# Kernel tuning notes

Hardware: AMD Instinct MI355X
Metric: run time of the kernel (lower is better)

Reference implementation:

```python
import jax, jax.numpy as jnp
import numpy as np

IN_CH = 1024   # backbone channels
N_T = 81       # n_targets (COCO classes + bg)
K = 7          # PSROI grid size
H = 100        # feature map height
WID = 100      # feature map width
R = 1024       # number of regions
S = 2          # bilinear sampling points per bin edge (PSROIAlign-style average)


def setup_inputs() -> dict:
    key = jax.random.key(0)
    k1, k2, k3 = jax.random.split(key, 3)
    x = jax.random.normal(k1, (IN_CH, H, WID), dtype=jnp.float32)
    # regions: fractional (i, j, h, w) = (center_y, center_x, height, width) in [0,1]
    regions = jax.random.uniform(k2, (R, 4), dtype=jnp.float32)
    conv_w = jax.random.normal(k3, (N_T * K * K, IN_CH), dtype=jnp.float32) * 0.02
    conv_b = jnp.zeros((N_T * K * K,), dtype=jnp.float32)
    return {"x": x, "regions": regions, "conv_w": conv_w, "conv_b": conv_b}


def _bilinear_pool(map_thw, ys, xs):
    """Average of bilinear samples of one bin's score map.

    map_thw: (T, H, W) score map for this (u, v) bin's channel group.
    ys: (R, S) sample row coords.  xs: (R, S) sample col coords.
    Returns (R, T): per-region average-pooled bin value.
    """
    Hm, Wm = map_thw.shape[1], map_thw.shape[2]
    ys = jnp.clip(ys, 0.0, Hm - 1)
    xs = jnp.clip(xs, 0.0, Wm - 1)
    y0 = jnp.floor(ys)
    x0 = jnp.floor(xs)
    y0i = y0.astype(jnp.int32)
    x0i = x0.astype(jnp.int32)
    y1i = jnp.minimum(y0i + 1, Hm - 1)
    x1i = jnp.minimum(x0i + 1, Wm - 1)
    wy1 = ys - y0
    wy0 = 1.0 - wy1
    wx1 = xs - x0
    wx0 = 1.0 - wx1

    def g(yi, xi):  # gather (T, R, S, S)
        return map_thw[:, yi[:, :, None], xi[:, None, :]]

    v = (g(y0i, x0i) * (wy0[:, :, None] * wx0[:, None, :])
         + g(y0i, x1i) * (wy0[:, :, None] * wx1[:, None, :])
         + g(y1i, x0i) * (wy1[:, :, None] * wx0[:, None, :])
         + g(y1i, x1i) * (wy1[:, :, None] * wx1[:, None, :]))
    return v.mean((2, 3)).T  # (R, T)


def reference(x, regions, conv_w, conv_b):
    # 1x1 conv score map: (n_targets*k^2, H, W)
    sm = jnp.einsum('oc,chw->ohw', conv_w, x) + conv_b[:, None, None]
    sm = sm.reshape(N_T, K, K, H, WID)  # (T, ky, kx, H, W) position-sensitive groups

    # region geometry (fractional center/size -> absolute feature-map coords)
    top = (regions[:, 0] - regions[:, 2] * 0.5) * H     # (R,)
    left = (regions[:, 1] - regions[:, 3] * 0.5) * WID  # (R,)
    bh = regions[:, 2] * H / K                          # bin height
    bw = regions[:, 3] * WID / K                        # bin width

    off = (jnp.arange(S, dtype=jnp.float32) + 0.5) / S  # (S,) sample offsets in bin
    bins = jnp.arange(K, dtype=jnp.float32)             # (K,)
    ys = top[:, None, None] + (bins[None, :, None] + off[None, None, :]) * bh[:, None, None]   # (R,K,S)
    xs = left[:, None, None] + (bins[None, :, None] + off[None, None, :]) * bw[:, None, None]  # (R,K,S)

    # vmap over the k x k position-sensitive bins; bin (u,v) reads channel group (:,u,v)
    inner = jax.vmap(_bilinear_pool, in_axes=(1, None, 1))  # over kx: sm axis, xs axis
    outer = jax.vmap(inner, in_axes=(1, 1, None))           # over ky: sm axis, ys axis
    pooled = outer(sm, ys, xs)  # (K, K, R, T)

    # pooled.mean(-1).mean(-1) over the k x k grid
    scores = pooled.mean((0, 1))  # (R, T)
    return scores
```

## Files before the change

### kernel.cpp

```cpp
#include <hip/hip_runtime.h>
#include <cstddef>

#define IN_CH 1024
#define NT    81
#define KGRID 7
#define NBINS 49
#define HH    100
#define WW    100
#define NPIX  (HH*WW)
#define NREG  1024
#define COLB  82
#define NCOL  (NBINS*COLB)
#define NPADW 4096
#define SBIN  84
#define SROWB (NBINS*SBIN)
#define NG    8
#define NSC   2560
#define PXB   ((NPIX + 31) / 32)
#define PXG   (PXB * (IN_CH / 128))
#define PREPG (PXG + NPADW)

typedef unsigned short ushortT;
typedef short bf16x8 __attribute__((ext_vector_type(8)));
typedef float f32x4  __attribute__((ext_vector_type(4)));

static __device__ __forceinline__ unsigned short f2bf(float f) {
    unsigned int u = __builtin_bit_cast(unsigned int, f);
    return (unsigned short)((u + 0x7fffu + ((u >> 16) & 1u)) >> 16);
}

static __device__ __forceinline__ void gld_lds16(const ushortT* g, ushortT* l) {
    __builtin_amdgcn_global_load_lds(
        (__attribute__((address_space(1))) void*)(unsigned long long)(uintptr_t)g,
        (__attribute__((address_space(3))) void*)(unsigned int)(unsigned long long)(uintptr_t)l,
        16, 0, 0);
}

__global__ __launch_bounds__(256) void prep_fused(const float* __restrict__ x,
                                                  ushortT* __restrict__ xbT,
                                                  const float* __restrict__ conv_w,
                                                  ushortT* __restrict__ Wr) {
    __shared__ float tile[128][33];
    const int tid = threadIdx.x;
    const int bid = blockIdx.x;
    if (bid < PXG) {
        const int p0 = (bid % PXB) * 32;
        const int c0 = (bid / PXB) * 128;
        const int pl = tid & 31;
        const int cg = tid >> 5;
        const int p = p0 + pl;
#pragma unroll
        for (int it = 0; it < 16; ++it) {
            const int c = it * 8 + cg;
            tile[c][pl] = (p < NPIX) ? x[(size_t)(c0 + c) * NPIX + p] : 0.0f;
        }
        __syncthreads();
#pragma unroll
        for (int pass = 0; pass < 2; ++pass) {
            const int pix = pass * 16 + (tid >> 4);
            const int cb  = (tid & 15) * 8;
            if (p0 + pix < NPIX) {
                uint4 pk;
                pk.x = (unsigned int)f2bf(tile[cb + 0][pix]) | ((unsigned int)f2bf(tile[cb + 1][pix]) << 16);
                pk.y = (unsigned int)f2bf(tile[cb + 2][pix]) | ((unsigned int)f2bf(tile[cb + 3][pix]) << 16);
                pk.z = (unsigned int)f2bf(tile[cb + 4][pix]) | ((unsigned int)f2bf(tile[cb + 5][pix]) << 16);
                pk.w = (unsigned int)f2bf(tile[cb + 6][pix]) | ((unsigned int)f2bf(tile[cb + 7][pix]) << 16);
                *(uint4*)(xbT + (size_t)(p0 + pix) * IN_CH + c0 + cb) = pk;
            }
        }
    } else {
        const int row = bid - PXG;
        const int bin = row / COLB;
        const int t   = row - bin * COLB;
        const int c   = tid * 4;
        uint2 pk; pk.x = 0; pk.y = 0;
        if (bin < NBINS && t < NT) {
            const float4 v = *(const float4*)(conv_w + ((size_t)(t * NBINS + bin)) * IN_CH + c);
            pk.x = (unsigned int)f2bf(v.x) | ((unsigned int)f2bf(v.y) << 16);
            pk.y = (unsigned int)f2bf(v.z) | ((unsigned int)f2bf(v.w) << 16);
        }
        *(uint2*)(Wr + (size_t)row * IN_CH + c) = pk;
    }
}

__global__ __launch_bounds__(256) void gemm_sm(const ushortT* __restrict__ xbT,
                                               const ushortT* __restrict__ Wr,
                                               unsigned char* __restrict__ sm,
                                               float* __restrict__ scales) {
    __shared__ ushortT a_lds[128 * 32];
    __shared__ ushortT b_lds[128 * 32];
    const int tid  = threadIdx.x;
    const int lane = tid & 63;
    const int w    = tid >> 6;
    const int wm   = w & 1;
    const int wn   = w >> 1;
    const int n0   = blockIdx.x * 128;
    const int p0   = blockIdx.y * 128;

    const int srow0 = w * 32 + (lane >> 2);
    const int scol  = (lane & 3) * 8;
    int ap0 = p0 + srow0;      if (ap0 > NPIX - 1) ap0 = NPIX - 1;
    int ap1 = p0 + srow0 + 16; if (ap1 > NPIX - 1) ap1 = NPIX - 1;
    const ushortT* ag0 = xbT + (size_t)ap0 * IN_CH + scol;
    const ushortT* ag1 = xbT + (size_t)ap1 * IN_CH + scol;
    const ushortT* bg0 = Wr + (size_t)(n0 + srow0) * IN_CH + scol;
    const ushortT* bg1 = Wr + (size_t)(n0 + srow0 + 16) * IN_CH + scol;
    ushortT* al0 = a_lds + (w * 32) * 32;
    ushortT* al1 = a_lds + (w * 32 + 16) * 32;
    ushortT* bl0 = b_lds + (w * 32) * 32;
    ushortT* bl1 = b_lds + (w * 32 + 16) * 32;

    const int m_lane = lane & 15;
    const int k0     = (lane >> 4) * 8;

    f32x4 acc[4][4];
#pragma unroll
    for (int mt = 0; mt < 4; ++mt)
#pragma unroll
        for (int nt = 0; nt < 4; ++nt) acc[mt][nt] = (f32x4){0.f, 0.f, 0.f, 0.f};

    for (int kc = 0; kc < IN_CH / 32; ++kc) {
        __syncthreads();
        gld_lds16(ag0, al0);
        gld_lds16(ag1, al1);
        gld_lds16(bg0, bl0);
        gld_lds16(bg1, bl1);
        ag0 += 32; ag1 += 32; bg0 += 32; bg1 += 32;
        __syncthreads();

        bf16x8 af[4], bf[4];
#pragma unroll
        for (int mt = 0; mt < 4; ++mt)
            af[mt] = *(const bf16x8*)(a_lds + (wm * 64 + mt * 16 + m_lane) * 32 + k0);
#pragma unroll
        for (int nt = 0; nt < 4; ++nt)
            bf[nt] = *(const bf16x8*)(b_lds + (wn * 64 + nt * 16 + m_lane) * 32 + k0);
#pragma unroll
        for (int mt = 0; mt < 4; ++mt)
#pragma unroll
            for (int nt = 0; nt < 4; ++nt)
                acc[mt][nt] = __builtin_amdgcn_mfma_f32_16x16x32_bf16(af[mt], bf[nt], acc[mt][nt], 0, 0, 0);
    }

    float am = 0.0f;
#pragma unroll
    for (int mt = 0; mt < 4; ++mt)
#pragma unroll
        for (int nt = 0; nt < 4; ++nt)
#pragma unroll
            for (int rg = 0; rg < 4; ++rg)
                am = fmaxf(am, fabsf(acc[mt][nt][rg]));
    __syncthreads();
    float* red = (float*)a_lds;
    red[tid] = am;
    __syncthreads();
#pragma unroll
    for (int s = 128; s > 0; s >>= 1) {
        if (tid < s) red[tid] = fmaxf(red[tid], red[tid + s]);
        __syncthreads();
    }
    const float amax = fmaxf(red[0], 1e-30f);
    const float inv  = 127.0f / amax;
    if (tid == 0) scales[blockIdx.y * 32 + blockIdx.x] = amax * (1.0f / 127.0f);

    const int prow_base = p0 + wm * 64 + (lane >> 4) * 4;
    const int ncol_base = n0 + wn * 64 + m_lane;
    int  coloff[4];
    bool cok[4];
#pragma unroll
    for (int nt = 0; nt < 4; ++nt) {
        const int n = ncol_base + nt * 16;
        cok[nt] = (n < NCOL);
        coloff[nt] = n + 2 * (n / COLB);
    }
#pragma unroll
    for (int mt = 0; mt < 4; ++mt) {
#pragma unroll
        for (int rg = 0; rg < 4; ++rg) {
            const int p = prow_base + mt * 16 + rg;
            if (p < NPIX) {
                unsigned char* rowp = sm + (size_t)p * SROWB;
#pragma unroll
                for (int nt = 0; nt < 4; ++nt)
                    if (cok[nt]) {
                        const int q = __float2int_rn(acc[mt][nt][rg] * inv);
                        rowp[coloff[nt]] = (unsigned char)(signed char)q;
                    }
            }
        }
    }
}

__global__ __launch_bounds__(256) void pool_kernel(const unsigned char* __restrict__ sm,
                                                   const float* __restrict__ scales,
                                                   const float* __restrict__ regions,
                                                   const float* __restrict__ conv_b,
                                                   float* __restrict__ out) {
    __shared__ int   rowo[28]; __shared__ float roww[28];
    __shared__ int   coli[28]; __shared__ float colw[28];
    __shared__ int   pofs[120];
    __shared__ float pw[120];
    __shared__ int   pptb[120];
    __shared__ int   pnb[120];
    __shared__ float part[40][100];
    const int tid = threadIdx.x;
    const int r = blockIdx.x;
    const int g = blockIdx.y;

    if (tid < 28) {
        const float4 reg = *(const float4*)(regions + (size_t)r * 4);
        const float top = (reg.x - reg.z * 0.5f) * (float)HH;
        const float bh  = reg.z * ((float)HH / (float)KGRID);
        const int u = tid >> 2, i = tid & 3;
        const int s = i >> 1, hi = i & 1;
        float y = top + ((float)u + ((float)s + 0.5f) * 0.5f) * bh;
        y = fminf(fmaxf(y, 0.0f), (float)(HH - 1));
        const float y0f = floorf(y);
        const int y0 = (int)y0f;
        const float wy1 = y - y0f;
        rowo[tid] = (hi ? min(y0 + 1, HH - 1) : y0) * WW;
        roww[tid] = hi ? wy1 : (1.0f - wy1);
    } else if (tid >= 32 && tid < 60) {
        const float4 reg = *(const float4*)(regions + (size_t)r * 4);
        const float left = (reg.y - reg.w * 0.5f) * (float)WW;
        const float bw   = reg.w * ((float)WW / (float)KGRID);
        const int idx = tid - 32;
        const int v = idx >> 2, j = idx & 3;
        const int s = j >> 1, hi = j & 1;
        float xx = left + ((float)v + ((float)s + 0.5f) * 0.5f) * bw;
        xx = fminf(fmaxf(xx, 0.0f), (float)(WW - 1));
        const float x0f = floorf(xx);
        const int x0 = (int)x0f;
        const float wx1 = xx - x0f;
        coli[idx] = hi ? min(x0 + 1, WW - 1) : x0;
        colw[idx] = hi ? wx1 : (1.0f - wx1);
    }
    __syncthreads();
    if (tid < 120) {
        if (tid < 98) {
            const int tt = g * 98 + tid;
            const int bin = tt >> 4, tap = tt & 15;
            const int u = bin / KGRID, v = bin - u * KGRID;
            const int i = tap >> 2, j = tap & 3;
            const int pix = rowo[u * 4 + i] + coli[v * 4 + j];
            pofs[tid] = pix * SROWB + bin * SBIN;
            pw[tid]   = roww[u * 4 + i] * colw[v * 4 + j] * (1.0f / 196.0f);
            pptb[tid] = (pix >> 7) * 32;
            pnb[tid]  = bin * COLB;
        } else {
            pofs[tid] = 0;
            pw[tid]   = 0.0f;
            pptb[tid] = 0;
            pnb[tid]  = 0;
        }
    }
    __syncthreads();

    const int lane = tid & 63, w = tid >> 6;
    const int sub  = lane / 6;
    const int cg   = lane - sub * 6;
    if (sub < 10) {
        const int str = w * 10 + sub;
        uint4 v[3];
#pragma unroll
        for (int it = 0; it < 3; ++it)
            v[it] = *(const uint4*)(sm + pofs[it * 40 + str] + cg * 16);

        float acc[16];
#pragma unroll
        for (int ch = 0; ch < 16; ++ch) acc[ch] = 0.0f;
#pragma unroll
        for (int it = 0; it < 3; ++it) {
            const int l  = it * 40 + str;
            const float wt = pw[l];
            const int nb  = pnb[l] + cg * 16;
            const int nt0 = nb >> 7;
            const int rr  = nb & 127;
            const float s0 = scales[pptb[l] + nt0];
            const float s1 = scales[pptb[l] + nt0 + 1];
            const float w0 = wt * s0, w1 = wt * s1;
            const unsigned int uu[4] = {v[it].x, v[it].y, v[it].z, v[it].w};
#pragma unroll
            for (int b = 0; b < 4; ++b) {
#pragma unroll
                for (int k = 0; k < 4; ++k) {
                    const int ch = b * 4 + k;
                    const int q = (int)(signed char)((uu[b] >> (k * 8)) & 0xff);
                    acc[ch] += ((rr < 128 - ch) ? w0 : w1) * (float)q;
                }
            }
        }
#pragma unroll
        for (int b = 0; b < 4; ++b) {
            float4 p4;
            p4.x = acc[b * 4]; p4.y = acc[b * 4 + 1];
            p4.z = acc[b * 4 + 2]; p4.w = acc[b * 4 + 3];
            *(float4*)&part[str][cg * 16 + b * 4] = p4;
        }
    }
    __syncthreads();
    if (tid < NT) {
        float vv = 0.f;
#pragma unroll
        for (int s = 0; s < 40; ++s) vv += part[s][tid];
        if (g == 0) {
            float bsum = 0.f;
            for (int bin = 0; bin < NBINS; ++bin) bsum += conv_b[tid * NBINS + bin];
            vv += bsum * (1.0f / (float)NBINS);
        }
        atomicAdd(out + (size_t)r * NT + tid, vv);
    }
}

__global__ __launch_bounds__(256) void xpose_kernel(const float* __restrict__ x,
                                                    float* __restrict__ xt) {
    __shared__ float tile[32][33];
    const int p0 = blockIdx.x * 32;
    const int c0 = blockIdx.y * 32;
    const int tx = threadIdx.x;
    const int ty = threadIdx.y;
#pragma unroll
    for (int k = 0; k < 32; k += 8) {
        const int p = p0 + tx;
        if (p < NPIX) tile[ty + k][tx] = x[(size_t)(c0 + ty + k) * NPIX + p];
    }
    __syncthreads();
#pragma unroll
    for (int k = 0; k < 32; k += 8) {
        const int p = p0 + ty + k;
        if (p < NPIX) xt[(size_t)p * IN_CH + (c0 + tx)] = tile[tx][ty + k];
    }
}

template <bool XPOSED>
__global__ __launch_bounds__(256) void psroi_kernel(
    const float* __restrict__ xsrc, const float* __restrict__ regions,
    const float* __restrict__ conv_w, const float* __restrict__ conv_b,
    float* __restrict__ out) {
    __shared__ float w_lds[32 * 96];
    __shared__ float g_lds[32 * 64];
    __shared__ int   rowoff[64][4];
    __shared__ float rowwf[64][4];
    __shared__ int   colidx[64][4];
    __shared__ float colwf[64][4];
    const int tid = threadIdx.x;
    const int bin = blockIdx.x >> 4;
    const int rg  = blockIdx.x & 15;
    const int u = bin / KGRID, v = bin % KGRID;
    const int r0 = rg * 64;
    if (tid < 64) {
        const float4 reg = *(const float4*)(regions + (size_t)(r0 + tid) * 4);
        const float top  = (reg.x - reg.z * 0.5f) * (float)HH;
        const float left = (reg.y - reg.w * 0.5f) * (float)WW;
        const float bh = reg.z * ((float)HH / (float)KGRID);
        const float bw = reg.w * ((float)WW / (float)KGRID);
        const float scale = 1.0f / 196.0f;
#pragma unroll
        for (int s = 0; s < 2; s++) {
            const float off = (s + 0.5f) * 0.5f;
            float yy = top + ((float)u + off) * bh;
            yy = fminf(fmaxf(yy, 0.0f), (float)(HH - 1));
            const float y0f = floorf(yy);
            const int y0 = (int)y0f;
            const float wy1 = yy - y0f;
            rowoff[tid][2 * s] = y0 * WW;
            rowoff[tid][2 * s + 1] = min(y0 + 1, HH - 1) * WW;
            rowwf[tid][2 * s] = (1.0f - wy1) * scale;
            rowwf[tid][2 * s + 1] = wy1 * scale;
            float xx = left + ((float)v + off) * bw;
            xx = fminf(fmaxf(xx, 0.0f), (float)(WW - 1));
            const float x0f = floorf(xx);
            const int x0 = (int)x0f;
            const float wx1 = xx - x0f;
            colidx[tid][2 * s] = x0;
            colidx[tid][2 * s + 1] = min(x0 + 1, WW - 1);
            colwf[tid][2 * s] = 1.0f - wx1;
            colwf[tid][2 * s + 1] = wx1;
        }
    }
    const int ri = tid & 15, tq = tid >> 4, rb = tid >> 2, cq = tid & 3;
    float acc[4][6];
#pragma unroll
    for (int m = 0; m < 4; m++)
#pragma unroll
        for (int k = 0; k < 6; k++) acc[m][k] = 0.0f;
    for (int chunk = 0; chunk < IN_CH / 32; chunk++) {
        const int c0 = chunk * 32;
        __syncthreads();
#pragma unroll
        for (int it = 0; it < 12; it++) {
            const int idx = it * 256 + tid;
            const int t = idx >> 5, c = idx & 31;
            float val = 0.0f;
            if (t < NT) val = conv_w[(size_t)(t * NBINS + bin) * IN_CH + c0 + c];
            w_lds[c * 96 + t] = val;
        }
        const int cbase = c0 + cq * 8;
        float g8[8];
#pragma unroll
        for (int cc = 0; cc < 8; cc++) g8[cc] = 0.0f;
#pragma unroll
        for (int i = 0; i < 4; i++) {
            const int ro = rowoff[rb][i];
            const float wy = rowwf[rb][i];
#pragma unroll
            for (int j = 0; j < 4; j++) {
                const int pix = ro + colidx[rb][j];
                const float wv = wy * colwf[rb][j];
                if (XPOSED) {
                    const float4* p = (const float4*)(xsrc + (size_t)pix * IN_CH + cbase);
                    const float4 a = p[0]; const float4 b = p[1];
                    g8[0] += wv * a.x; g8[1] += wv * a.y; g8[2] += wv * a.z; g8[3] += wv * a.w;
                    g8[4] += wv * b.x; g8[5] += wv * b.y; g8[6] += wv * b.z; g8[7] += wv * b.w;
                } else {
#pragma unroll
                    for (int cc = 0; cc < 8; cc++)
                        g8[cc] += wv * xsrc[(size_t)(cbase + cc) * NPIX + pix];
                }
            }
        }
#pragma unroll
        for (int cc = 0; cc < 8; cc++) g_lds[(cq * 8 + cc) * 64 + rb] = g8[cc];
        __syncthreads();
#pragma unroll 4
        for (int c = 0; c < 32; c++) {
            float wv[6];
#pragma unroll
            for (int k = 0; k < 6; k++) wv[k] = w_lds[c * 96 + tq * 6 + k];
            const float4 gq = *(const float4*)&g_lds[c * 64 + ri * 4];
            const float gm[4] = {gq.x, gq.y, gq.z, gq.w};
#pragma unroll
            for (int m = 0; m < 4; m++)
#pragma unroll
                for (int k = 0; k < 6; k++) acc[m][k] += gm[m] * wv[k];
        }
    }
    const float invK2 = 1.0f / 49.0f;
#pragma unroll
    for (int k = 0; k < 6; k++) {
        const int t = tq * 6 + k;
        if (t < NT) {
            const float bterm = conv_b[t * NBINS + bin] * invK2;
#pragma unroll
            for (int m = 0; m < 4; m++) {
                const int rr = r0 + ri * 4 + m;
                atomicAdd(&out[(size_t)rr * NT + t], acc[m][k] + bterm);
            }
        }
    }
}

extern "C" void kernel_launch(void* const* d_in, const int* in_sizes, int n_in,
                              void* d_out, int out_size, void* d_ws, size_t ws_size,
                              hipStream_t stream) {
    const float* x       = (const float*)d_in[0];
    const float* regions = (const float*)d_in[1];
    const float* conv_w  = (const float*)d_in[2];
    const float* conv_b  = (const float*)d_in[3];
    float* out = (float*)d_out;

    const size_t sz_xbT = (size_t)NPIX * IN_CH * 2;
    const size_t sz_Wr  = (size_t)NPADW * IN_CH * 2;
    const size_t sz_sm  = (size_t)NPIX * SROWB + 256;
    const size_t sz_sc  = (size_t)NSC * sizeof(float);
    const size_t need   = sz_xbT + sz_Wr + sz_sm + sz_sc;

    if (ws_size >= need) {
        ushortT* xbT = (ushortT*)d_ws;
        ushortT* Wr  = (ushortT*)((char*)d_ws + sz_xbT);
        unsigned char* sm = (unsigned char*)d_ws + sz_xbT + sz_Wr;
        float* scales = (float*)((char*)d_ws + sz_xbT + sz_Wr + sz_sm);
        hipMemsetAsync(out, 0, (size_t)out_size * sizeof(float), stream);
        prep_fused<<<dim3(PREPG), 256, 0, stream>>>(x, xbT, conv_w, Wr);
        gemm_sm<<<dim3(NPADW / 128, (NPIX + 127) / 128), 256, 0, stream>>>(xbT, Wr, sm, scales);
        pool_kernel<<<dim3(NREG, NG), 256, 0, stream>>>(sm, scales, regions, conv_b, out);
    } else {
        hipMemsetAsync(out, 0, (size_t)out_size * sizeof(float), stream);
        const size_t xt_bytes = (size_t)NPIX * IN_CH * sizeof(float);
        const dim3 mainGrid(NBINS * 16);
        if (ws_size >= xt_bytes) {
            float* xt = (float*)d_ws;
            xpose_kernel<<<dim3((NPIX + 31) / 32, IN_CH / 32), dim3(32, 8), 0, stream>>>(x, xt);
            psroi_kernel<true><<<mainGrid, 256, 0, stream>>>(xt, regions, conv_w, conv_b, out);
        } else {
            psroi_kernel<false><<<mainGrid, 256, 0, stream>>>(x, regions, conv_w, conv_b, out);
        }
    }
}
```

Measured before the change: 235.0 us.

## Rewrite bf16 GEMM as 256x256 double-buffered tile with swizzled LDS and grid remap

Replaces the 128x128 single-buffered MFMA GEMM with a 512-thread, 256x256-tile kernel. It uses double-buffered LDS with XOR-swizzled addressing, a K step of 64, staggered global-to-LDS prefetch overlapped with MFMA phases, s_setprio around the MFMA groups, and a remapped block order. The goal is to cut global traffic per FLOP, hide load latency and avoid LDS bank conflicts. Quantization scale granularity stays at 128x128 sub-tiles, so the scales layout remains compatible with the pool kernel. Larger tiles mean 640 blocks and more waste at the tile edges, and occupancy depends on the larger LDS footprint.

```diff
diff --git a/kernel.cpp b/kernel.cpp
--- a/kernel.cpp
+++ b/kernel.cpp
@@ -20,6 +20,10 @@
 #define PXG   (PXB * (IN_CH / 128))
 #define PREPG (PXG + NPADW)
 
+#define GM_T  40
+#define GN_T  16
+#define NKT   16
+
 typedef unsigned short ushortT;
 typedef short bf16x8 __attribute__((ext_vector_type(8)));
 typedef float f32x4  __attribute__((ext_vector_type(4)));
@@ -34,6 +38,12 @@
         (__attribute__((address_space(1))) void*)(unsigned long long)(uintptr_t)g,
         (__attribute__((address_space(3))) void*)(unsigned int)(unsigned long long)(uintptr_t)l,
         16, 0, 0);
+}
+
+static __device__ __forceinline__ void barf() {
+    asm volatile("" ::: "memory");
+    __builtin_amdgcn_s_barrier();
+    asm volatile("" ::: "memory");
 }
 
 __global__ __launch_bounds__(256) void prep_fused(const float* __restrict__ x,
@@ -83,112 +93,184 @@
     }
 }
 
-__global__ __launch_bounds__(256) void gemm_sm(const ushortT* __restrict__ xbT,
-                                               const ushortT* __restrict__ Wr,
-                                               unsigned char* __restrict__ sm,
-                                               float* __restrict__ scales) {
-    __shared__ ushortT a_lds[128 * 32];
-    __shared__ ushortT b_lds[128 * 32];
+__global__ __launch_bounds__(512, 2) void gemm_sm(const ushortT* __restrict__ xbT,
+                                                  const ushortT* __restrict__ Wr,
+                                                  unsigned char* __restrict__ sm,
+                                                  float* __restrict__ scales) {
+    __shared__ ushortT lA[2][16384];
+    __shared__ ushortT lB[2][16384];
+
     const int tid  = threadIdx.x;
     const int lane = tid & 63;
     const int w    = tid >> 6;
     const int wm   = w & 1;
     const int wn   = w >> 1;
-    const int n0   = blockIdx.x * 128;
-    const int p0   = blockIdx.y * 128;
-
-    const int srow0 = w * 32 + (lane >> 2);
-    const int scol  = (lane & 3) * 8;
-    int ap0 = p0 + srow0;      if (ap0 > NPIX - 1) ap0 = NPIX - 1;
-    int ap1 = p0 + srow0 + 16; if (ap1 > NPIX - 1) ap1 = NPIX - 1;
-    const ushortT* ag0 = xbT + (size_t)ap0 * IN_CH + scol;
-    const ushortT* ag1 = xbT + (size_t)ap1 * IN_CH + scol;
-    const ushortT* bg0 = Wr + (size_t)(n0 + srow0) * IN_CH + scol;
-    const ushortT* bg1 = Wr + (size_t)(n0 + srow0 + 16) * IN_CH + scol;
-    ushortT* al0 = a_lds + (w * 32) * 32;
-    ushortT* al1 = a_lds + (w * 32 + 16) * 32;
-    ushortT* bl0 = b_lds + (w * 32) * 32;
-    ushortT* bl1 = b_lds + (w * 32 + 16) * 32;
-
-    const int m_lane = lane & 15;
-    const int k0     = (lane >> 4) * 8;
-
-    f32x4 acc[4][4];
-#pragma unroll
-    for (int mt = 0; mt < 4; ++mt)
-#pragma unroll
-        for (int nt = 0; nt < 4; ++nt) acc[mt][nt] = (f32x4){0.f, 0.f, 0.f, 0.f};
-
-    for (int kc = 0; kc < IN_CH / 32; ++kc) {
-        __syncthreads();
-        gld_lds16(ag0, al0);
-        gld_lds16(ag1, al1);
-        gld_lds16(bg0, bl0);
-        gld_lds16(bg1, bl1);
-        ag0 += 32; ag1 += 32; bg0 += 32; bg1 += 32;
-        __syncthreads();
-
-        bf16x8 af[4], bf[4];
+
+    const int bid   = blockIdx.x;
+    const int sw    = (bid & 7) * 80 + (bid >> 3);
+    const int mtile = sw >> 4;
+    const int ntile = sw & 15;
+    const int p0 = mtile * 256;
+    const int n0 = ntile * 256;
+
+    const int l3   = lane >> 3;
+    const int srco = ((lane & 7) ^ l3) << 3;
+    const int w2   = w * 2;
+
+    const ushortT* gA[2][2];
+    const ushortT* gB[2][2];
+    int dstA[2][2], dstB[2][2];
+#pragma unroll
+    for (int h = 0; h < 2; ++h)
+#pragma unroll
+        for (int it = 0; it < 2; ++it) {
+            const int hr = (w2 + it) * 8 + l3;
+            int p = p0 + h * 128 + hr; if (p > NPIX - 1) p = NPIX - 1;
+            gA[h][it] = xbT + (size_t)p * IN_CH + srco;
+            gB[h][it] = Wr + (size_t)(n0 + h * 128 + hr) * IN_CH + srco;
+            dstA[h][it] = h * 8192 + (w2 + it) * 512 + lane * 8;
+            dstB[h][it] = dstA[h][it];
+        }
+
+#define STAGE_A(bb, h, T) { gld_lds16(gA[h][0] + (size_t)(T) * 64, &lA[bb][dstA[h][0]]); \
+                            gld_lds16(gA[h][1] + (size_t)(T) * 64, &lA[bb][dstA[h][1]]); }
+#define STAGE_B(bb, h, T) { gld_lds16(gB[h][0] + (size_t)(T) * 64, &lB[bb][dstB[h][0]]); \
+                            gld_lds16(gB[h][1] + (size_t)(T) * 64, &lB[bb][dstB[h][1]]); }
+
+    const int m_l = lane & 15;
+    const int kq  = lane >> 4;
+    const int ph0 = ((kq) ^ (lane & 7)) << 3;
+    const int ph1 = ((4 + kq) ^ (lane & 7)) << 3;
+    const int arow = (wm * 128 + m_l) * 64;
+    const int brow = (wn * 64 + m_l) * 64;
+
+#define RD_A(bb, mq) { _Pragma("unroll") for (int mt = 0; mt < 4; ++mt) { \
+        const int ro = arow + ((mq) * 64 + mt * 16) * 64; \
+        af[mt][0] = *(const bf16x8*)(&lA[bb][ro + ph0]); \
+        af[mt][1] = *(const bf16x8*)(&lA[bb][ro + ph1]); } }
+#define RD_B(dst, bb, nq) { _Pragma("unroll") for (int nt = 0; nt < 2; ++nt) { \
+        const int ro = brow + ((nq) * 32 + nt * 16) * 64; \
+        dst[nt][0] = *(const bf16x8*)(&lB[bb][ro + ph0]); \
+        dst[nt][1] = *(const bf16x8*)(&lB[bb][ro + ph1]); } }
+#define MM(mq, B, nq) { _Pragma("unroll") for (int mt = 0; mt < 4; ++mt) \
+        _Pragma("unroll") for (int nt = 0; nt < 2; ++nt) { \
+        acc[mq][mt][nq][nt] = __builtin_amdgcn_mfma_f32_16x16x32_bf16(af[mt][0], B[nt][0], acc[mq][mt][nq][nt], 0, 0, 0); \
+        acc[mq][mt][nq][nt] = __builtin_amdgcn_mfma_f32_16x16x32_bf16(af[mt][1], B[nt][1], acc[mq][mt][nq][nt], 0, 0, 0); } }
+
+    f32x4 acc[2][4][2][2];
+#pragma unroll
+    for (int a = 0; a < 2; ++a)
+#pragma unroll
+        for (int b = 0; b < 4; ++b)
+#pragma unroll
+            for (int c = 0; c < 2; ++c)
+#pragma unroll
+                for (int d = 0; d < 2; ++d) acc[a][b][c][d] = (f32x4){0.f, 0.f, 0.f, 0.f};
+
+    bf16x8 af[4][2], bf0[2][2], bf1[2][2];
+
+    STAGE_A(0, 0, 0); STAGE_A(0, 1, 0); STAGE_B(0, 0, 0); STAGE_B(0, 1, 0);
+    STAGE_A(1, 0, 1); STAGE_A(1, 1, 1);
+    asm volatile("s_waitcnt vmcnt(4)" ::: "memory");
+    __builtin_amdgcn_s_barrier();
+    asm volatile("" ::: "memory");
+
+#pragma unroll 2
+    for (int kt = 0; kt < NKT; ++kt) {
+        const int b = kt & 1;
+        RD_A(b, 0);
+        RD_B(bf0, b, 0);
+        if (kt < NKT - 1) STAGE_B(b ^ 1, 0, kt + 1);
+        barf();
+        __builtin_amdgcn_s_setprio(1);
+        MM(0, bf0, 0);
+        __builtin_amdgcn_s_setprio(0);
+        barf();
+        RD_B(bf1, b, 1);
+        if (kt < NKT - 1) STAGE_B(b ^ 1, 1, kt + 1);
+        barf();
+        __builtin_amdgcn_s_setprio(1);
+        MM(0, bf1, 1);
+        __builtin_amdgcn_s_setprio(0);
+        barf();
+        RD_A(b, 1);
+        barf();
+        __builtin_amdgcn_s_setprio(1);
+        MM(1, bf1, 1);
+        __builtin_amdgcn_s_setprio(0);
+        barf();
+        __builtin_amdgcn_s_setprio(1);
+        MM(1, bf0, 0);
+        __builtin_amdgcn_s_setprio(0);
+        if (kt < NKT - 2) {
+            STAGE_A(b, 0, kt + 2); STAGE_A(b, 1, kt + 2);
+            asm volatile("s_waitcnt vmcnt(4)" ::: "memory");
+        } else {
+            asm volatile("s_waitcnt vmcnt(0)" ::: "memory");
+        }
+        __builtin_amdgcn_s_barrier();
+        asm volatile("" ::: "memory");
+    }
+
+    __syncthreads();
+    float am = 0.0f;
+#pragma unroll
+    for (int mq = 0; mq < 2; ++mq)
 #pragma unroll
         for (int mt = 0; mt < 4; ++mt)
-            af[mt] = *(const bf16x8*)(a_lds + (wm * 64 + mt * 16 + m_lane) * 32 + k0);
-#pragma unroll
-        for (int nt = 0; nt < 4; ++nt)
-            bf[nt] = *(const bf16x8*)(b_lds + (wn * 64 + nt * 16 + m_lane) * 32 + k0);
+#pragma unroll
+            for (int nq = 0; nq < 2; ++nq)
+#pragma unroll
+                for (int nt = 0; nt < 2; ++nt)
+#pragma unroll
+                    for (int rg = 0; rg < 4; ++rg)
+                        am = fmaxf(am, fabsf(acc[mq][mt][nq][nt][rg]));
+#pragma unroll
+    for (int off = 32; off > 0; off >>= 1) am = fmaxf(am, __shfl_xor(am, off));
+    float* red = (float*)lA;
+    if (lane == 0) red[w] = am;
+    __syncthreads();
+    const float qam = fmaxf(fmaxf(red[w], red[w ^ 2]), 1e-30f);
+    const float inv = 127.0f / qam;
+    if (lane == 0 && (wn & 1) == 0)
+        scales[(mtile * 2 + wm) * 32 + ntile * 2 + (wn >> 1)] = qam * (1.0f / 127.0f);
+
+    const int prow0 = p0 + wm * 128 + kq * 4;
+    const int ncol0 = n0 + wn * 64 + m_l;
+    int  coloff[2][2];
+    bool cok[2][2];
+#pragma unroll
+    for (int nq = 0; nq < 2; ++nq)
+#pragma unroll
+        for (int nt = 0; nt < 2; ++nt) {
+            const int n = ncol0 + nq * 32 + nt * 16;
+            cok[nq][nt] = (n < NCOL);
+            coloff[nq][nt] = n + 2 * (n / COLB);
+        }
+#pragma unroll
+    for (int mq = 0; mq < 2; ++mq)
 #pragma unroll
         for (int mt = 0; mt < 4; ++mt)
 #pragma unroll
-            for (int nt = 0; nt < 4; ++nt)
-                acc[mt][nt] = __builtin_amdgcn_mfma_f32_16x16x32_bf16(af[mt], bf[nt], acc[mt][nt], 0, 0, 0);
-    }
-
-    float am = 0.0f;
-#pragma unroll
-    for (int mt = 0; mt < 4; ++mt)
-#pragma unroll
-        for (int nt = 0; nt < 4; ++nt)
-#pragma unroll
-            for (int rg = 0; rg < 4; ++rg)
-                am = fmaxf(am, fabsf(acc[mt][nt][rg]));
-    __syncthreads();
-    float* red = (float*)a_lds;
-    red[tid] = am;
-    __syncthreads();
-#pragma unroll
-    for (int s = 128; s > 0; s >>= 1) {
-        if (tid < s) red[tid] = fmaxf(red[tid], red[tid + s]);
-        __syncthreads();
-    }
-    const float amax = fmaxf(red[0], 1e-30f);
-    const float inv  = 127.0f / amax;
-    if (tid == 0) scales[blockIdx.y * 32 + blockIdx.x] = amax * (1.0f / 127.0f);
-
-    const int prow_base = p0 + wm * 64 + (lane >> 4) * 4;
-    const int ncol_base = n0 + wn * 64 + m_lane;
-    int  coloff[4];
-    bool cok[4];
-#pragma unroll
-    for (int nt = 0; nt < 4; ++nt) {
-        const int n = ncol_base + nt * 16;
-        cok[nt] = (n < NCOL);
-        coloff[nt] = n + 2 * (n / COLB);
-    }
-#pragma unroll
-    for (int mt = 0; mt < 4; ++mt) {
-#pragma unroll
-        for (int rg = 0; rg < 4; ++rg) {
-            const int p = prow_base + mt * 16 + rg;
-            if (p < NPIX) {
-                unsigned char* rowp = sm + (size_t)p * SROWB;
-#pragma unroll
-                for (int nt = 0; nt < 4; ++nt)
-                    if (cok[nt]) {
-                        const int q = __float2int_rn(acc[mt][nt][rg] * inv);
-                        rowp[coloff[nt]] = (unsigned char)(signed char)q;
-                    }
+            for (int rg = 0; rg < 4; ++rg) {
+                const int p = prow0 + mq * 64 + mt * 16 + rg;
+                if (p < NPIX) {
+                    unsigned char* rowp = sm + (size_t)p * SROWB;
+#pragma unroll
+                    for (int nq = 0; nq < 2; ++nq)
+#pragma unroll
+                        for (int nt = 0; nt < 2; ++nt)
+                            if (cok[nq][nt]) {
+                                const int q = __float2int_rn(acc[mq][mt][nq][nt][rg] * inv);
+                                rowp[coloff[nq][nt]] = (unsigned char)(signed char)q;
+                            }
+                }
             }
-        }
-    }
+#undef STAGE_A
+#undef STAGE_B
+#undef RD_A
+#undef RD_B
+#undef MM
 }
 
 __global__ __launch_bounds__(256) void pool_kernel(const unsigned char* __restrict__ sm,
@@ -472,7 +554,7 @@
         float* scales = (float*)((char*)d_ws + sz_xbT + sz_Wr + sz_sm);
         hipMemsetAsync(out, 0, (size_t)out_size * sizeof(float), stream);
         prep_fused<<<dim3(PREPG), 256, 0, stream>>>(x, xbT, conv_w, Wr);
-        gemm_sm<<<dim3(NPADW / 128, (NPIX + 127) / 128), 256, 0, stream>>>(xbT, Wr, sm, scales);
+        gemm_sm<<<dim3(GM_T * GN_T), 512, 0, stream>>>(xbT, Wr, sm, scales);
         pool_kernel<<<dim3(NREG, NG), 256, 0, stream>>>(sm, scales, regions, conv_b, out);
     } else {
         hipMemsetAsync(out, 0, (size_t)out_size * sizeof(float), stream);
```

Measured after the change: 231.1 us. About the same (-1.7%).
